# Performance work log

Measured on AMD Instinct MI355X. Metric: run time of the kernel, lower is better.

The kernel has to match this reference:

```python
import jax, jax.numpy as jnp
import numpy as np
from jax import lax

N_GRAPHS = 256
N_NODES = 128      # nodes per graph (fixed-size batching)
N_TPLT = 16
N_TPLT_NODES = 10
N_FEAT = 128
AVG_DEG = 8
EPS = 0.1          # entropic regularization for the GW solver
OUTER_ITERS = 5    # outer mirror-descent (entropic GW) iterations
SINKHORN_ITERS = 20


def setup_inputs() -> dict:
    key = jax.random.key(0)
    k1, k2, k3, k4, k5 = jax.random.split(key, 5)
    x = jax.random.normal(k1, (N_GRAPHS * N_NODES, N_FEAT), jnp.float32)
    # per-graph random edges with global node ids (PyG convention)
    n_e = N_NODES * AVG_DEG
    src = jax.random.randint(k2, (N_GRAPHS, n_e), 0, N_NODES)
    dst = jax.random.randint(k3, (N_GRAPHS, n_e), 0, N_NODES)
    off = (jnp.arange(N_GRAPHS) * N_NODES)[:, None]
    edge_index = jnp.stack([(src + off).reshape(-1), (dst + off).reshape(-1)]).astype(jnp.int32)
    batch = jnp.repeat(jnp.arange(N_GRAPHS, dtype=jnp.int32), N_NODES)
    # template parameters (symmetric uniform adjacencies, normal features, zero q0 -> uniform weights)
    A0 = jax.random.uniform(k4, (N_TPLT, N_TPLT_NODES, N_TPLT_NODES), jnp.float32)
    tplt_adjacencies = 0.5 * (A0 + jnp.swapaxes(A0, 1, 2))
    tplt_features = jax.random.normal(k5, (N_TPLT, N_TPLT_NODES, N_FEAT), jnp.float32)
    q0 = jnp.zeros((N_TPLT, N_TPLT_NODES), jnp.float32)
    return {"x": x, "edge_index": edge_index, "batch": batch,
            "tplt_adjacencies": tplt_adjacencies, "tplt_features": tplt_features, "q0": q0}


def _gw_distances(C1, C2, p, q):
    # C1: [B,N,N] graph adjacencies, C2: [T,M,M] templates, p: [N], q: [T,M]
    # square-loss GW decomposition (Peyre et al.): f1=a^2, f2=b^2, h1=a, h2=2b
    B, N = C1.shape[0], C1.shape[1]
    T, M = C2.shape[0], C2.shape[1]
    f1p = jnp.einsum('bij,j->bi', C1 * C1, p)          # [B,N]
    f2q = jnp.einsum('tij,tj->ti', C2 * C2, q)         # [T,M]
    constC = f1p[:, None, :, None] + f2q[None, :, None, :]  # [B,T,N,M]

    def tens(P):
        # constC - h1(C1) P h2(C2)^T
        cross = jnp.einsum('bik,btkm,tjm->btij', C1, P, 2.0 * C2)
        return constC - cross

    P0 = jnp.broadcast_to(p[None, None, :, None] * q[None, :, None, :], (B, T, N, M))

    def outer(P, _):
        cost = 2.0 * tens(P)                     # GW gradient
        K = jnp.exp(-cost / EPS)                 # [B,T,N,M]
        u0 = jnp.ones((B, T, N), K.dtype)
        v0 = jnp.ones((B, T, M), K.dtype)

        def inner(carry, _):
            u, v = carry
            u = p[None, None, :] / jnp.einsum('btnm,btm->btn', K, v)
            v = q[None, :, :] / jnp.einsum('btnm,btn->btm', K, u)
            return (u, v), None

        (u, v), _ = lax.scan(inner, (u0, v0), None, length=SINKHORN_ITERS)
        P = u[..., :, None] * K * v[..., None, :]
        return P, None

    P, _ = lax.scan(outer, P0, None, length=OUTER_ITERS)
    return jnp.sum(tens(P) * P, axis=(2, 3))     # [B,T]


def reference(x, edge_index, batch, tplt_adjacencies, tplt_features, q0):
    # q = softmax(q0, dim=1): template node weights
    q = jax.nn.softmax(q0, axis=1)
    # dense per-graph adjacency from the sparse edge list
    g = batch[edge_index[0]]
    src = edge_index[0] - g * N_NODES
    dst = edge_index[1] - g * N_NODES
    C1 = jnp.zeros((N_GRAPHS, N_NODES, N_NODES), x.dtype)
    C1 = C1.at[g, src, dst].set(1.0)
    C1 = jnp.maximum(C1, jnp.swapaxes(C1, 1, 2))  # undirected
    p = jnp.full((N_NODES,), 1.0 / N_NODES, x.dtype)  # uniform graph node weights
    # fused=False: pure Gromov-Wasserstein, node features are not used
    return _gw_distances(C1, tplt_adjacencies, p, q)
```

## Files before the change

### kernel.cpp

```cpp
#include <hip/hip_runtime.h>

#define NGRAPH 256
#define NN     128
#define NT     16
#define NM     10
#define OUTER_IT 5
#define SINK_IT  20
#define COST_SCALE 20.0f

typedef unsigned long long u64;

template <int CTRL>
__device__ __forceinline__ float dpp_add(float a) {
  int t = __builtin_amdgcn_update_dpp(0, __float_as_int(a), CTRL, 0xf, 0xf, true);
  return a + __int_as_float(t);
}
__device__ __forceinline__ float allsum16(float x) {
  x = dpp_add<0xB1>(x);
  x = dpp_add<0x4E>(x);
  x = dpp_add<0x141>(x);
  x = dpp_add<0x140>(x);
  return x;
}

__global__ __launch_bounds__(64, 1)
void tgw_kernel(const int* __restrict__ ei,
                const float* __restrict__ tadj,
                const float* __restrict__ q0g,
                float* __restrict__ out,
                int E, int ne) {
  const int lane = threadIdx.x;
  const int g    = lane >> 4;
  const int sub  = lane & 15;
  const int b    = blockIdx.x >> 2;
  const int tb   = (blockIdx.x & 3) * 4;

  __shared__ unsigned adj[NN][4];
  __shared__ __align__(16) float Pls[4][129][12];
  __shared__ __align__(16) float C2s[4][NM][12];
  __shared__ float q0s[4][NM];

  for (int i = lane; i < NN * 4; i += 64) (&adj[0][0])[i] = 0u;
  for (int i = lane; i < 4 * NM * NM; i += 64) {
    int tt = i / (NM * NM), rem = i % (NM * NM);
    C2s[tt][rem / NM][rem % NM] = tadj[(tb + tt) * NM * NM + rem];
  }
  for (int i = lane; i < 4 * NM; i += 64)
    q0s[i / NM][i % NM] = q0g[tb * NM + i];
  __syncthreads();

  const int* srcp = ei;
  const int* dstp = ei + E;
  const int ebase = b * ne;
  for (int e = lane; e < ne; e += 64) {
    int s = srcp[ebase + e] & (NN - 1);
    int d = dstp[ebase + e] & (NN - 1);
    atomicOr(&adj[s][d >> 5], 1u << (d & 31));
    atomicOr(&adj[d][s >> 5], 1u << (s & 31));
  }
  __syncthreads();

  float qv[NM], f2q[NM];
  {
    float mx = q0s[g][0];
    #pragma unroll
    for (int j = 1; j < NM; ++j) mx = fmaxf(mx, q0s[g][j]);
    float s = 0.f;
    #pragma unroll
    for (int j = 0; j < NM; ++j) { qv[j] = __expf(q0s[g][j] - mx); s += qv[j]; }
    float inv = __builtin_amdgcn_rcpf(s);
    #pragma unroll
    for (int j = 0; j < NM; ++j) qv[j] *= inv;
  }
  #pragma unroll
  for (int j = 0; j < NM; ++j) {
    float a = 0.f;
    #pragma unroll
    for (int m = 0; m < NM; ++m) { float c = C2s[g][j][m]; a = fmaf(c * c, qv[m], a); }
    f2q[j] = a;
  }

  const float pw = 1.0f / 128.0f;
  float f1p[8];
  #pragma unroll
  for (int jj = 0; jj < 8; ++jj) {
    uint4 mm = *(const uint4*)&adj[sub + 16 * jj][0];
    u64 m0 = mm.x | ((u64)mm.y << 32), m1 = mm.z | ((u64)mm.w << 32);
    f1p[jj] = (float)(__popcll(m0) + __popcll(m1)) * pw;
  }

  auto gather4 = [&](int jj0, float S4[4][NM]) {
    #pragma unroll
    for (int c = 0; c < 4; ++c) {
      const int r = sub + 16 * (jj0 + c);
      uint4 mm = *(const uint4*)&adj[r][0];
      u64 m0 = mm.x | ((u64)mm.y << 32), m1 = mm.z | ((u64)mm.w << 32);
      float S[NM];
      #pragma unroll
      for (int j = 0; j < NM; ++j) S[j] = 0.f;
      while (m0) {
        int k = (int)__builtin_ctzll(m0); m0 &= m0 - 1;
        const float* row = &Pls[g][k][0];
        float4 a = *(const float4*)row;
        float4 bb = *(const float4*)(row + 4);
        float2 cc = *(const float2*)(row + 8);
        S[0] += a.x;  S[1] += a.y;  S[2] += a.z;  S[3] += a.w;
        S[4] += bb.x; S[5] += bb.y; S[6] += bb.z; S[7] += bb.w;
        S[8] += cc.x; S[9] += cc.y;
      }
      while (m1) {
        int k = 64 + (int)__builtin_ctzll(m1); m1 &= m1 - 1;
        const float* row = &Pls[g][k][0];
        float4 a = *(const float4*)row;
        float4 bb = *(const float4*)(row + 4);
        float2 cc = *(const float2*)(row + 8);
        S[0] += a.x;  S[1] += a.y;  S[2] += a.z;  S[3] += a.w;
        S[4] += bb.x; S[5] += bb.y; S[6] += bb.z; S[7] += bb.w;
        S[8] += cc.x; S[9] += cc.y;
      }
      #pragma unroll
      for (int j = 0; j < NM; ++j) S4[c][j] = S[j];
    }
  };

  float Kc[8][NM], vv[NM], uu[8];

  for (int o = 0; o < OUTER_IT; ++o) {
    #pragma unroll
    for (int half = 0; half < 2; ++half) {
      const int jj0 = half * 4;
      float S4[4][NM];
      if (o == 0) {
        #pragma unroll
        for (int c = 0; c < 4; ++c)
          #pragma unroll
          for (int j = 0; j < NM; ++j) S4[c][j] = f1p[jj0 + c] * qv[j];
      } else {
        gather4(jj0, S4);
      }
      #pragma unroll
      for (int j = 0; j < NM; ++j) {
        const float* c2r = &C2s[g][j][0];
        float4 ca = *(const float4*)c2r;
        float4 cb = *(const float4*)(c2r + 4);
        float2 cd = *(const float2*)(c2r + 8);
        #pragma unroll
        for (int c = 0; c < 4; ++c) {
          float cr = S4[c][0] * ca.x;
          cr = fmaf(S4[c][1], ca.y, cr); cr = fmaf(S4[c][2], ca.z, cr);
          cr = fmaf(S4[c][3], ca.w, cr); cr = fmaf(S4[c][4], cb.x, cr);
          cr = fmaf(S4[c][5], cb.y, cr); cr = fmaf(S4[c][6], cb.z, cr);
          cr = fmaf(S4[c][7], cb.w, cr); cr = fmaf(S4[c][8], cd.x, cr);
          cr = fmaf(S4[c][9], cd.y, cr);
          float tv = f1p[jj0 + c] + f2q[j] - 2.f * cr;
          Kc[jj0 + c][j] = __expf(-COST_SCALE * tv);
        }
      }
    }

    #pragma unroll
    for (int j = 0; j < NM; ++j) vv[j] = 1.f;
    for (int it = 0; it < SINK_IT; ++it) {
      #pragma unroll
      for (int jj = 0; jj < 8; ++jj) {
        float d = Kc[jj][0] * vv[0];
        #pragma unroll
        for (int j = 1; j < NM; ++j) d = fmaf(Kc[jj][j], vv[j], d);
        uu[jj] = pw * __builtin_amdgcn_rcpf(d);
      }
      #pragma unroll
      for (int j = 0; j < NM; ++j) {
        float w = Kc[0][j] * uu[0];
        #pragma unroll
        for (int jj = 1; jj < 8; ++jj) w = fmaf(Kc[jj][j], uu[jj], w);
        float cs = allsum16(w);
        vv[j] = qv[j] * __builtin_amdgcn_rcpf(cs);
      }
    }

    __syncthreads();
    #pragma unroll
    for (int jj = 0; jj < 8; ++jj) {
      const int r = sub + 16 * jj;
      float x[NM];
      #pragma unroll
      for (int j = 0; j < NM; ++j) x[j] = uu[jj] * Kc[jj][j] * vv[j];
      float* row = &Pls[g][r][0];
      *(float4*)row       = make_float4(x[0], x[1], x[2], x[3]);
      *(float4*)(row + 4) = make_float4(x[4], x[5], x[6], x[7]);
      *(float2*)(row + 8) = make_float2(x[8], x[9]);
    }
    __syncthreads();
  }

  float acc = 0.f;
  #pragma unroll
  for (int half = 0; half < 2; ++half) {
    const int jj0 = half * 4;
    float S4[4][NM];
    gather4(jj0, S4);
    #pragma unroll
    for (int j = 0; j < NM; ++j) {
      const float* c2r = &C2s[g][j][0];
      float4 ca = *(const float4*)c2r;
      float4 cb = *(const float4*)(c2r + 4);
      float2 cd = *(const float2*)(c2r + 8);
      #pragma unroll
      for (int c = 0; c < 4; ++c) {
        const int jj = jj0 + c;
        float cr = S4[c][0] * ca.x;
        cr = fmaf(S4[c][1], ca.y, cr); cr = fmaf(S4[c][2], ca.z, cr);
        cr = fmaf(S4[c][3], ca.w, cr); cr = fmaf(S4[c][4], cb.x, cr);
        cr = fmaf(S4[c][5], cb.y, cr); cr = fmaf(S4[c][6], cb.z, cr);
        cr = fmaf(S4[c][7], cb.w, cr); cr = fmaf(S4[c][8], cd.x, cr);
        cr = fmaf(S4[c][9], cd.y, cr);
        float tv = f1p[jj] + f2q[j] - 2.f * cr;
        float Pv = uu[jj] * Kc[jj][j] * vv[j];
        acc = fmaf(tv, Pv, acc);
      }
    }
  }
  float total = allsum16(acc);
  if (sub == 0) out[b * NT + tb + g] = total;
}

extern "C" void kernel_launch(void* const* d_in, const int* in_sizes, int n_in,
                              void* d_out, int out_size, void* d_ws, size_t ws_size,
                              hipStream_t stream) {
  const int* ei   = (const int*)d_in[1];
  const float* c2 = (const float*)d_in[3];
  const float* q0 = (const float*)d_in[5];
  float* out      = (float*)d_out;
  const int E  = in_sizes[1] / 2;
  const int ne = E / NGRAPH;
  tgw_kernel<<<dim3(NGRAPH * 4), dim3(64), 0, stream>>>(ei, c2, q0, out, E, ne);
}
```

Measured before the change: 226.9 us.

## Split work as two templates per block with 32 lanes each

Each block now handles two templates instead of four, with 32 lanes per template so each lane owns 4 graph nodes instead of 8. The grid doubles to 2048 blocks and launch bounds allow two waves per SIMD, cutting per-lane register arrays and serial Sinkhorn work. The column reduction becomes a 32-lane sum using a ds_swizzle step. In exchange, each graph's adjacency is rebuilt twice as often and the edge atomics are duplicated.

```diff
diff --git a/kernel.cpp b/kernel.cpp
--- a/kernel.cpp
+++ b/kernel.cpp
@@ -15,38 +15,38 @@
   int t = __builtin_amdgcn_update_dpp(0, __float_as_int(a), CTRL, 0xf, 0xf, true);
   return a + __int_as_float(t);
 }
-__device__ __forceinline__ float allsum16(float x) {
+__device__ __forceinline__ float allsum32(float x) {
   x = dpp_add<0xB1>(x);
   x = dpp_add<0x4E>(x);
   x = dpp_add<0x141>(x);
   x = dpp_add<0x140>(x);
-  return x;
-}
-
-__global__ __launch_bounds__(64, 1)
+  int sw = __builtin_amdgcn_ds_swizzle(__float_as_int(x), 0x401F);
+  return x + __int_as_float(sw);
+}
+
+__global__ __launch_bounds__(64, 2)
 void tgw_kernel(const int* __restrict__ ei,
                 const float* __restrict__ tadj,
                 const float* __restrict__ q0g,
                 float* __restrict__ out,
                 int E, int ne) {
   const int lane = threadIdx.x;
-  const int g    = lane >> 4;
-  const int sub  = lane & 15;
-  const int b    = blockIdx.x >> 2;
-  const int tb   = (blockIdx.x & 3) * 4;
-
-  __shared__ unsigned adj[NN][4];
-  __shared__ __align__(16) float Pls[4][129][12];
-  __shared__ __align__(16) float C2s[4][NM][12];
-  __shared__ float q0s[4][NM];
+  const int p    = lane >> 5;
+  const int sub  = lane & 31;
+  const int b    = blockIdx.x >> 3;
+  const int t0   = (blockIdx.x & 7) * 2;
+
+  __shared__ __align__(16) unsigned adj[NN][4];
+  __shared__ __align__(16) float Pls[2][NN][12];
+  __shared__ __align__(16) float C2s[2][NM][12];
+  __shared__ float q0s[2][NM];
 
   for (int i = lane; i < NN * 4; i += 64) (&adj[0][0])[i] = 0u;
-  for (int i = lane; i < 4 * NM * NM; i += 64) {
+  for (int i = lane; i < 2 * NM * NM; i += 64) {
     int tt = i / (NM * NM), rem = i % (NM * NM);
-    C2s[tt][rem / NM][rem % NM] = tadj[(tb + tt) * NM * NM + rem];
-  }
-  for (int i = lane; i < 4 * NM; i += 64)
-    q0s[i / NM][i % NM] = q0g[tb * NM + i];
+    C2s[tt][rem / NM][rem % NM] = tadj[(t0 + tt) * NM * NM + rem];
+  }
+  if (lane < 2 * NM) q0s[lane / NM][lane % NM] = q0g[t0 * NM + lane];
   __syncthreads();
 
   const int* srcp = ei;
@@ -62,12 +62,12 @@
 
   float qv[NM], f2q[NM];
   {
-    float mx = q0s[g][0];
-    #pragma unroll
-    for (int j = 1; j < NM; ++j) mx = fmaxf(mx, q0s[g][j]);
+    float mx = q0s[p][0];
+    #pragma unroll
+    for (int j = 1; j < NM; ++j) mx = fmaxf(mx, q0s[p][j]);
     float s = 0.f;
     #pragma unroll
-    for (int j = 0; j < NM; ++j) { qv[j] = __expf(q0s[g][j] - mx); s += qv[j]; }
+    for (int j = 0; j < NM; ++j) { qv[j] = __expf(q0s[p][j] - mx); s += qv[j]; }
     float inv = __builtin_amdgcn_rcpf(s);
     #pragma unroll
     for (int j = 0; j < NM; ++j) qv[j] *= inv;
@@ -76,152 +76,141 @@
   for (int j = 0; j < NM; ++j) {
     float a = 0.f;
     #pragma unroll
-    for (int m = 0; m < NM; ++m) { float c = C2s[g][j][m]; a = fmaf(c * c, qv[m], a); }
+    for (int m = 0; m < NM; ++m) { float c = C2s[p][j][m]; a = fmaf(c * c, qv[m], a); }
     f2q[j] = a;
   }
 
   const float pw = 1.0f / 128.0f;
-  float f1p[8];
+  float f1p[4];
   #pragma unroll
-  for (int jj = 0; jj < 8; ++jj) {
-    uint4 mm = *(const uint4*)&adj[sub + 16 * jj][0];
+  for (int c = 0; c < 4; ++c) {
+    uint4 mm = *(const uint4*)&adj[sub + 32 * c][0];
     u64 m0 = mm.x | ((u64)mm.y << 32), m1 = mm.z | ((u64)mm.w << 32);
-    f1p[jj] = (float)(__popcll(m0) + __popcll(m1)) * pw;
-  }
-
-  auto gather4 = [&](int jj0, float S4[4][NM]) {
-    #pragma unroll
-    for (int c = 0; c < 4; ++c) {
-      const int r = sub + 16 * (jj0 + c);
-      uint4 mm = *(const uint4*)&adj[r][0];
-      u64 m0 = mm.x | ((u64)mm.y << 32), m1 = mm.z | ((u64)mm.w << 32);
-      float S[NM];
-      #pragma unroll
-      for (int j = 0; j < NM; ++j) S[j] = 0.f;
-      while (m0) {
-        int k = (int)__builtin_ctzll(m0); m0 &= m0 - 1;
-        const float* row = &Pls[g][k][0];
-        float4 a = *(const float4*)row;
-        float4 bb = *(const float4*)(row + 4);
-        float2 cc = *(const float2*)(row + 8);
-        S[0] += a.x;  S[1] += a.y;  S[2] += a.z;  S[3] += a.w;
-        S[4] += bb.x; S[5] += bb.y; S[6] += bb.z; S[7] += bb.w;
-        S[8] += cc.x; S[9] += cc.y;
-      }
-      while (m1) {
-        int k = 64 + (int)__builtin_ctzll(m1); m1 &= m1 - 1;
-        const float* row = &Pls[g][k][0];
-        float4 a = *(const float4*)row;
-        float4 bb = *(const float4*)(row + 4);
-        float2 cc = *(const float2*)(row + 8);
-        S[0] += a.x;  S[1] += a.y;  S[2] += a.z;  S[3] += a.w;
-        S[4] += bb.x; S[5] += bb.y; S[6] += bb.z; S[7] += bb.w;
-        S[8] += cc.x; S[9] += cc.y;
-      }
-      #pragma unroll
-      for (int j = 0; j < NM; ++j) S4[c][j] = S[j];
+    f1p[c] = (float)(__popcll(m0) + __popcll(m1)) * pw;
+  }
+
+  const float* Pbase = &Pls[p][0][0];
+  auto gatherRow = [&](int r, float* S) {
+    uint4 mm = *(const uint4*)&adj[r][0];
+    u64 m0 = mm.x | ((u64)mm.y << 32), m1 = mm.z | ((u64)mm.w << 32);
+    #pragma unroll
+    for (int j = 0; j < NM; ++j) S[j] = 0.f;
+    while (m0) {
+      int k = (int)__builtin_ctzll(m0); m0 &= m0 - 1;
+      const float* row = Pbase + k * 12;
+      float4 a = *(const float4*)row;
+      float4 bb = *(const float4*)(row + 4);
+      float2 cc = *(const float2*)(row + 8);
+      S[0] += a.x;  S[1] += a.y;  S[2] += a.z;  S[3] += a.w;
+      S[4] += bb.x; S[5] += bb.y; S[6] += bb.z; S[7] += bb.w;
+      S[8] += cc.x; S[9] += cc.y;
+    }
+    while (m1) {
+      int k = 64 + (int)__builtin_ctzll(m1); m1 &= m1 - 1;
+      const float* row = Pbase + k * 12;
+      float4 a = *(const float4*)row;
+      float4 bb = *(const float4*)(row + 4);
+      float2 cc = *(const float2*)(row + 8);
+      S[0] += a.x;  S[1] += a.y;  S[2] += a.z;  S[3] += a.w;
+      S[4] += bb.x; S[5] += bb.y; S[6] += bb.z; S[7] += bb.w;
+      S[8] += cc.x; S[9] += cc.y;
     }
   };
 
-  float Kc[8][NM], vv[NM], uu[8];
+  float Kc[4][NM], vv[NM], uu[4];
 
   for (int o = 0; o < OUTER_IT; ++o) {
-    #pragma unroll
-    for (int half = 0; half < 2; ++half) {
-      const int jj0 = half * 4;
-      float S4[4][NM];
-      if (o == 0) {
+    float S4[4][NM];
+    if (o == 0) {
+      #pragma unroll
+      for (int c = 0; c < 4; ++c)
         #pragma unroll
-        for (int c = 0; c < 4; ++c)
-          #pragma unroll
-          for (int j = 0; j < NM; ++j) S4[c][j] = f1p[jj0 + c] * qv[j];
-      } else {
-        gather4(jj0, S4);
-      }
-      #pragma unroll
-      for (int j = 0; j < NM; ++j) {
-        const float* c2r = &C2s[g][j][0];
-        float4 ca = *(const float4*)c2r;
-        float4 cb = *(const float4*)(c2r + 4);
-        float2 cd = *(const float2*)(c2r + 8);
-        #pragma unroll
-        for (int c = 0; c < 4; ++c) {
-          float cr = S4[c][0] * ca.x;
-          cr = fmaf(S4[c][1], ca.y, cr); cr = fmaf(S4[c][2], ca.z, cr);
-          cr = fmaf(S4[c][3], ca.w, cr); cr = fmaf(S4[c][4], cb.x, cr);
-          cr = fmaf(S4[c][5], cb.y, cr); cr = fmaf(S4[c][6], cb.z, cr);
-          cr = fmaf(S4[c][7], cb.w, cr); cr = fmaf(S4[c][8], cd.x, cr);
-          cr = fmaf(S4[c][9], cd.y, cr);
-          float tv = f1p[jj0 + c] + f2q[j] - 2.f * cr;
-          Kc[jj0 + c][j] = __expf(-COST_SCALE * tv);
-        }
-      }
-    }
-
-    #pragma unroll
-    for (int j = 0; j < NM; ++j) vv[j] = 1.f;
-    for (int it = 0; it < SINK_IT; ++it) {
-      #pragma unroll
-      for (int jj = 0; jj < 8; ++jj) {
-        float d = Kc[jj][0] * vv[0];
-        #pragma unroll
-        for (int j = 1; j < NM; ++j) d = fmaf(Kc[jj][j], vv[j], d);
-        uu[jj] = pw * __builtin_amdgcn_rcpf(d);
-      }
-      #pragma unroll
-      for (int j = 0; j < NM; ++j) {
-        float w = Kc[0][j] * uu[0];
-        #pragma unroll
-        for (int jj = 1; jj < 8; ++jj) w = fmaf(Kc[jj][j], uu[jj], w);
-        float cs = allsum16(w);
-        vv[j] = qv[j] * __builtin_amdgcn_rcpf(cs);
-      }
-    }
-
-    __syncthreads();
-    #pragma unroll
-    for (int jj = 0; jj < 8; ++jj) {
-      const int r = sub + 16 * jj;
-      float x[NM];
-      #pragma unroll
-      for (int j = 0; j < NM; ++j) x[j] = uu[jj] * Kc[jj][j] * vv[j];
-      float* row = &Pls[g][r][0];
-      *(float4*)row       = make_float4(x[0], x[1], x[2], x[3]);
-      *(float4*)(row + 4) = make_float4(x[4], x[5], x[6], x[7]);
-      *(float2*)(row + 8) = make_float2(x[8], x[9]);
-    }
-    __syncthreads();
-  }
-
-  float acc = 0.f;
-  #pragma unroll
-  for (int half = 0; half < 2; ++half) {
-    const int jj0 = half * 4;
-    float S4[4][NM];
-    gather4(jj0, S4);
+        for (int j = 0; j < NM; ++j) S4[c][j] = f1p[c] * qv[j];
+    } else {
+      #pragma unroll
+      for (int c = 0; c < 4; ++c) gatherRow(sub + 32 * c, S4[c]);
+    }
     #pragma unroll
     for (int j = 0; j < NM; ++j) {
-      const float* c2r = &C2s[g][j][0];
+      const float* c2r = &C2s[p][j][0];
       float4 ca = *(const float4*)c2r;
       float4 cb = *(const float4*)(c2r + 4);
       float2 cd = *(const float2*)(c2r + 8);
       #pragma unroll
       for (int c = 0; c < 4; ++c) {
-        const int jj = jj0 + c;
         float cr = S4[c][0] * ca.x;
         cr = fmaf(S4[c][1], ca.y, cr); cr = fmaf(S4[c][2], ca.z, cr);
         cr = fmaf(S4[c][3], ca.w, cr); cr = fmaf(S4[c][4], cb.x, cr);
         cr = fmaf(S4[c][5], cb.y, cr); cr = fmaf(S4[c][6], cb.z, cr);
         cr = fmaf(S4[c][7], cb.w, cr); cr = fmaf(S4[c][8], cd.x, cr);
         cr = fmaf(S4[c][9], cd.y, cr);
-        float tv = f1p[jj] + f2q[j] - 2.f * cr;
-        float Pv = uu[jj] * Kc[jj][j] * vv[j];
+        float tv = f1p[c] + f2q[j] - 2.f * cr;
+        Kc[c][j] = __expf(-COST_SCALE * tv);
+      }
+    }
+
+    #pragma unroll
+    for (int j = 0; j < NM; ++j) vv[j] = 1.f;
+    for (int it = 0; it < SINK_IT; ++it) {
+      #pragma unroll
+      for (int c = 0; c < 4; ++c) {
+        float d = Kc[c][0] * vv[0];
+        #pragma unroll
+        for (int j = 1; j < NM; ++j) d = fmaf(Kc[c][j], vv[j], d);
+        uu[c] = pw * __builtin_amdgcn_rcpf(d);
+      }
+      #pragma unroll
+      for (int j = 0; j < NM; ++j) {
+        float w = Kc[0][j] * uu[0];
+        w = fmaf(Kc[1][j], uu[1], w);
+        w = fmaf(Kc[2][j], uu[2], w);
+        w = fmaf(Kc[3][j], uu[3], w);
+        float cs = allsum32(w);
+        vv[j] = qv[j] * __builtin_amdgcn_rcpf(cs);
+      }
+    }
+
+    __syncthreads();
+    #pragma unroll
+    for (int c = 0; c < 4; ++c) {
+      float x[NM];
+      #pragma unroll
+      for (int j = 0; j < NM; ++j) x[j] = uu[c] * Kc[c][j] * vv[j];
+      float* row = &Pls[p][sub + 32 * c][0];
+      *(float4*)row       = make_float4(x[0], x[1], x[2], x[3]);
+      *(float4*)(row + 4) = make_float4(x[4], x[5], x[6], x[7]);
+      *(float2*)(row + 8) = make_float2(x[8], x[9]);
+    }
+    __syncthreads();
+  }
+
+  float acc = 0.f;
+  {
+    float S4[4][NM];
+    #pragma unroll
+    for (int c = 0; c < 4; ++c) gatherRow(sub + 32 * c, S4[c]);
+    #pragma unroll
+    for (int j = 0; j < NM; ++j) {
+      const float* c2r = &C2s[p][j][0];
+      float4 ca = *(const float4*)c2r;
+      float4 cb = *(const float4*)(c2r + 4);
+      float2 cd = *(const float2*)(c2r + 8);
+      #pragma unroll
+      for (int c = 0; c < 4; ++c) {
+        float cr = S4[c][0] * ca.x;
+        cr = fmaf(S4[c][1], ca.y, cr); cr = fmaf(S4[c][2], ca.z, cr);
+        cr = fmaf(S4[c][3], ca.w, cr); cr = fmaf(S4[c][4], cb.x, cr);
+        cr = fmaf(S4[c][5], cb.y, cr); cr = fmaf(S4[c][6], cb.z, cr);
+        cr = fmaf(S4[c][7], cb.w, cr); cr = fmaf(S4[c][8], cd.x, cr);
+        cr = fmaf(S4[c][9], cd.y, cr);
+        float tv = f1p[c] + f2q[j] - 2.f * cr;
+        float Pv = uu[c] * Kc[c][j] * vv[j];
         acc = fmaf(tv, Pv, acc);
       }
     }
   }
-  float total = allsum16(acc);
-  if (sub == 0) out[b * NT + tb + g] = total;
+  float total = allsum32(acc);
+  if (sub == 0) out[b * NT + t0 + p] = total;
 }
 
 extern "C" void kernel_launch(void* const* d_in, const int* in_sizes, int n_in,
@@ -233,5 +222,5 @@
   float* out      = (float*)d_out;
   const int E  = in_sizes[1] / 2;
   const int ne = E / NGRAPH;
-  tgw_kernel<<<dim3(NGRAPH * 4), dim3(64), 0, stream>>>(ei, c2, q0, out, E, ne);
-}
+  tgw_kernel<<<dim3(NGRAPH * 8), dim3(64), 0, stream>>>(ei, c2, q0, out, E, ne);
+}
```

Result: faster. 203.8 us (-10.2%).
